# Performance work log

Hardware: AMD Instinct MI355X
Metric: run time of the kernel (lower is better)

## Reference

```python
import jax, jax.numpy as jnp
import numpy as np

B, I, N, T = 256, 1024, 1024, 100
TAU = 20.0
NUM_WEIGHT_BITS = 8  # -> numLsbBits = 8 - (8-1) = 1
VMAX = 2.0**23 - 1.0
VMIN = -(2.0**23) + 1.0


def setup_inputs() -> dict:
    key = jax.random.key(0)
    k1, k2, k3 = jax.random.split(key, 3)
    input_spikes = jax.random.randint(k1, (B, I, T), 0, 2, dtype=jnp.int32)  # binary spikes
    weight = jax.random.normal(k2, (N, I), dtype=jnp.float32)
    bias = jax.random.normal(k3, (N,), dtype=jnp.float32)
    return {"input_spikes": input_spikes, "weight": weight, "bias": bias}


def _quantize(weight, bias):
    # scale_factor = 255 / max|w|; int() truncates toward zero
    scale = 255.0 / jnp.max(jnp.abs(weight))
    qw = jnp.trunc(weight * scale)
    # (x >> 1) << 1 with arithmetic shift == floor(x/2)*2
    qw = jnp.floor(qw / 2.0) * 2.0
    qw = qw * 64.0
    qb = jnp.trunc(bias * scale) * 64.0
    vth = jnp.trunc(1.0 * scale) * 64.0  # vTh option default = 1.0
    return qw, qb, vth


def reference(input_spikes, weight, bias):
    qw, qb, vth = _quantize(weight, bias)
    decay = float(int(4096 - np.exp(-1.0 / TAU) * 4096))  # int truncation, = 199
    keep = (4096.0 - decay) / 4096.0
    spikes_t = jnp.transpose(input_spikes, (2, 0, 1)).astype(jnp.float32)  # [T,B,I]

    def step(v, s):
        wi = s @ qw.T                       # [B,N]
        v = v * keep + wi + qb              # soft LIF update
        v = jnp.clip(v, VMIN, VMAX)
        spike = (v >= vth).astype(jnp.float32)
        v = jnp.where(v > vth, v - vth, v)  # soft reset (strict >)
        return v, spike

    v0 = jnp.zeros((B, N), jnp.float32)
    _, spikes = jax.lax.scan(step, v0, spikes_t)       # [T,B,N]
    out = jnp.transpose(spikes, (1, 2, 0))             # [B,N,T]
    # delay == 1: prepend zeros, drop last two -> length T-1
    out = jnp.concatenate([jnp.zeros((B, N, 1), jnp.float32), out[..., : T - 2]], axis=-1)
    return out
```

## Files before the change

kernel.cpp:

```cpp
#include <hip/hip_runtime.h>
#include <hip/hip_bf16.h>
#include <stdint.h>

#define B_ 256
#define I_ 1024
#define N_ 1024
#define T_ 100
#define TP_ 128
#define TOUT 99
#define BN_ 64
#define KEEP (3897.0f/4096.0f)
#define VMAXF 8388607.0f
#define VMINF (-8388607.0f)

typedef __attribute__((ext_vector_type(8))) short short8;
typedef __attribute__((ext_vector_type(4))) float f32x4;

#define WS_MAX 0
#define WS_QB  4096
#define WS_QW  8192
#define WS_ST  (8192 + 2*1024*1024)

__global__ void maxabs_k(const float* __restrict__ w, unsigned* __restrict__ mx) {
  float m = 0.f;
  int stride = gridDim.x * blockDim.x;
  for (int i = blockIdx.x * blockDim.x + threadIdx.x; i < N_ * I_; i += stride)
    m = fmaxf(m, fabsf(w[i]));
  #pragma unroll
  for (int off = 32; off > 0; off >>= 1)
    m = fmaxf(m, __shfl_xor(m, off));
  if ((threadIdx.x & 63) == 0) atomicMax(mx, __float_as_uint(m));
}

__global__ void quant_k(const float* __restrict__ w, const float* __restrict__ bias,
                        const unsigned* __restrict__ mx,
                        unsigned short* __restrict__ qw, float* __restrict__ qb) {
  const float scale = 255.0f / __uint_as_float(*mx);
  int gid = blockIdx.x * blockDim.x + threadIdx.x;
  int stride = gridDim.x * blockDim.x;
  for (int idx = gid; idx < N_ * I_; idx += stride) {
    float q = truncf(__fmul_rn(w[idx], scale));
    q = floorf(q * 0.5f) * 2.0f;
    q = q * 64.0f;
    qw[idx] = (unsigned short)(__float_as_uint(q) >> 16);
  }
  if (gid < N_)
    qb[gid] = truncf(__fmul_rn(bias[gid], scale)) * 64.0f;
}

__global__ void spk_transpose_k(const int* __restrict__ spk, unsigned short* __restrict__ st) {
  __shared__ unsigned short tile[TP_][66];
  const int b = blockIdx.y;
  const int i0 = blockIdx.x * 64;
  for (int idx = threadIdx.x; idx < 28 * 64; idx += 256)
    tile[100 + (idx >> 6)][idx & 63] = 0;
  for (int idx = threadIdx.x; idx < 64 * 25; idx += 256) {
    int il = idx / 25, c = idx - il * 25;
    const int4 v = *(const int4*)(spk + ((size_t)(b * I_ + i0 + il)) * T_ + 4 * c);
    int t = 4 * c;
    tile[t + 0][il] = (unsigned short)(v.x ? 0x3F80 : 0);
    tile[t + 1][il] = (unsigned short)(v.y ? 0x3F80 : 0);
    tile[t + 2][il] = (unsigned short)(v.z ? 0x3F80 : 0);
    tile[t + 3][il] = (unsigned short)(v.w ? 0x3F80 : 0);
  }
  __syncthreads();
  for (int idx = threadIdx.x; idx < 128 * 32; idx += 256) {
    int t = idx >> 5, c = idx & 31;
    unsigned u = *(const unsigned*)&tile[t][c * 2];
    *(unsigned*)(st + ((size_t)b * TP_ + t) * I_ + i0 + c * 2) = u;
  }
}

__global__ __launch_bounds__(256, 4)
void gemm_scan_k(const unsigned short* __restrict__ st,
                 const unsigned short* __restrict__ qw,
                 const float* __restrict__ qb,
                 const unsigned* __restrict__ mx,
                 float* __restrict__ out) {
  __shared__ __align__(16) char smem[128 * 65 * 4];

  const int bid = blockIdx.x;
  const int swz = (bid & 7) * 512 + (bid >> 3);
  const int b  = swz >> 4;
  const int n0 = (swz & 15) * BN_;

  const int tid  = threadIdx.x;
  const int lane = tid & 63;
  const int wv   = tid >> 6;
  const int wr = wv >> 1, wc = wv & 1;
  const int lrow = lane & 15;
  const int lk16 = (lane >> 4) * 16;

  f32x4 acc[4][2];
  #pragma unroll
  for (int i = 0; i < 4; ++i)
    #pragma unroll
    for (int j = 0; j < 2; ++j)
      acc[i][j] = (f32x4){0.f, 0.f, 0.f, 0.f};

  const char* stB = (const char*)st + (size_t)b * TP_ * I_ * 2;
  const char* qwB = (const char*)qw + (size_t)n0 * I_ * 2;

  const char* gA[4]; const char* gB[2];
  #pragma unroll
  for (int j = 0; j < 4; ++j) {
    int lin = (j * 256 + tid) * 16;
    int row = lin >> 7, cb = lin & 127;
    gA[j] = stB + (size_t)row * 2048 + (cb ^ ((row & 7) << 4));
  }
  #pragma unroll
  for (int j = 0; j < 2; ++j) {
    int lin = (j * 256 + tid) * 16;
    int row = lin >> 7, cb = lin & 127;
    gB[j] = qwB + (size_t)row * 2048 + (cb ^ ((row & 7) << 4));
  }

  int offA[4][2], offB[2][2];
  #pragma unroll
  for (int mi = 0; mi < 4; ++mi) {
    int row = wr * 64 + mi * 16 + lrow;
    #pragma unroll
    for (int kk = 0; kk < 2; ++kk)
      offA[mi][kk] = row * 128 + ((kk * 64 + lk16) ^ ((row & 7) << 4));
  }
  #pragma unroll
  for (int ni = 0; ni < 2; ++ni) {
    int row = wc * 32 + ni * 16 + lrow;
    #pragma unroll
    for (int kk = 0; kk < 2; ++kk)
      offB[ni][kk] = 16384 + row * 128 + ((kk * 64 + lk16) ^ ((row & 7) << 4));
  }

  for (int ks = 0; ks < 16; ++ks) {
    const int g = ks * 128;
    #pragma unroll
    for (int j = 0; j < 4; ++j)
      __builtin_amdgcn_global_load_lds(
          (const __attribute__((address_space(1))) void*)(gA[j] + g),
          (__attribute__((address_space(3))) void*)(smem + j * 4096 + wv * 1024), 16, 0, 0);
    #pragma unroll
    for (int j = 0; j < 2; ++j)
      __builtin_amdgcn_global_load_lds(
          (const __attribute__((address_space(1))) void*)(gB[j] + g),
          (__attribute__((address_space(3))) void*)(smem + 16384 + j * 4096 + wv * 1024), 16, 0, 0);
    __syncthreads();

    #pragma unroll
    for (int kk = 0; kk < 2; ++kk) {
      short8 af[4], bf[2];
      #pragma unroll
      for (int mi = 0; mi < 4; ++mi) af[mi] = *(const short8*)(smem + offA[mi][kk]);
      #pragma unroll
      for (int ni = 0; ni < 2; ++ni) bf[ni] = *(const short8*)(smem + offB[ni][kk]);
      #pragma unroll
      for (int mi = 0; mi < 4; ++mi)
        #pragma unroll
        for (int ni = 0; ni < 2; ++ni)
          acc[mi][ni] = __builtin_amdgcn_mfma_f32_16x16x32_bf16(af[mi], bf[ni], acc[mi][ni], 0, 0, 0);
    }
    __syncthreads();
  }

  float* WI = (float*)smem;
  #pragma unroll
  for (int mi = 0; mi < 4; ++mi) {
    int row = wr * 64 + mi * 16 + (lane >> 4) * 4;
    #pragma unroll
    for (int ni = 0; ni < 2; ++ni) {
      int col = wc * 32 + ni * 16 + (lane & 15);
      #pragma unroll
      for (int j = 0; j < 4; ++j)
        WI[(row + j) * 65 + col] = acc[mi][ni][j];
    }
  }
  __syncthreads();

  if (tid < BN_) {
    const float scale = 255.0f / __uint_as_float(*mx);
    const float vth = truncf(scale) * 64.0f;
    const float qbn = qb[n0 + tid];
    float v = 0.f;
    float* orow = out + (size_t)(b * N_ + n0 + tid) * TOUT;
    orow[0] = 0.0f;
    for (int t = 0; t < 98; ++t) {
      float wi = WI[t * 65 + tid];
      v = __fadd_rn(__fadd_rn(__fmul_rn(v, KEEP), wi), qbn);
      v = fminf(fmaxf(v, VMINF), VMAXF);
      orow[t + 1] = (v >= vth) ? 1.0f : 0.0f;
      if (v > vth) v = __fsub_rn(v, vth);
    }
  }
}

extern "C" void kernel_launch(void* const* d_in, const int* in_sizes, int n_in,
                              void* d_out, int out_size, void* d_ws, size_t ws_size,
                              hipStream_t stream) {
  const int*   spikes = (const int*)d_in[0];
  const float* weight = (const float*)d_in[1];
  const float* bias   = (const float*)d_in[2];
  float* out = (float*)d_out;
  char* ws = (char*)d_ws;

  unsigned*       mx = (unsigned*)(ws + WS_MAX);
  float*          qb = (float*)(ws + WS_QB);
  unsigned short* qw = (unsigned short*)(ws + WS_QW);
  unsigned short* st = (unsigned short*)(ws + WS_ST);

  hipMemsetAsync(mx, 0, 4, stream);
  maxabs_k<<<256, 256, 0, stream>>>(weight, mx);
  quant_k<<<1024, 256, 0, stream>>>(weight, bias, mx, qw, qb);
  spk_transpose_k<<<dim3(16, 256), 256, 0, stream>>>(spikes, st);
  gemm_scan_k<<<4096, 256, 0, stream>>>(st, qw, qb, mx, out);
}
```

Before: 315.5 us.

## Switch spike GEMM to int8 MFMA with double-buffered LDS staging

Stores the quantized weights as int8 (floor(q/2)) and the spikes as int8 0/1, then runs the batched spike GEMM with i32 16x16x64 int8 MFMA and rescales by 128 in the epilogue. This halves the bytes for the weight and spike operands and doubles the K-step per MFMA. The main loop also double-buffers LDS, prefetching the next K tile while computing the current one, using explicit waitcnt and barriers. Integer accumulation stays exact because the products are small, but the hand-placed waitcnt and barrier ordering is fragile.

```diff
diff --git a/kernel.cpp b/kernel.cpp
--- a/kernel.cpp
+++ b/kernel.cpp
@@ -1,5 +1,4 @@
 #include <hip/hip_runtime.h>
-#include <hip/hip_bf16.h>
 #include <stdint.h>
 
 #define B_ 256
@@ -13,13 +12,12 @@
 #define VMAXF 8388607.0f
 #define VMINF (-8388607.0f)
 
-typedef __attribute__((ext_vector_type(8))) short short8;
-typedef __attribute__((ext_vector_type(4))) float f32x4;
+typedef __attribute__((ext_vector_type(4))) int i32x4;
 
 #define WS_MAX 0
 #define WS_QB  4096
 #define WS_QW  8192
-#define WS_ST  (8192 + 2*1024*1024)
+#define WS_ST  (8192 + 1024*1024 + 4096)
 
 __global__ void maxabs_k(const float* __restrict__ w, unsigned* __restrict__ mx) {
   float m = 0.f;
@@ -34,22 +32,20 @@
 
 __global__ void quant_k(const float* __restrict__ w, const float* __restrict__ bias,
                         const unsigned* __restrict__ mx,
-                        unsigned short* __restrict__ qw, float* __restrict__ qb) {
+                        signed char* __restrict__ qw, float* __restrict__ qb) {
   const float scale = 255.0f / __uint_as_float(*mx);
   int gid = blockIdx.x * blockDim.x + threadIdx.x;
   int stride = gridDim.x * blockDim.x;
   for (int idx = gid; idx < N_ * I_; idx += stride) {
-    float q = truncf(__fmul_rn(w[idx], scale));
-    q = floorf(q * 0.5f) * 2.0f;
-    q = q * 64.0f;
-    qw[idx] = (unsigned short)(__float_as_uint(q) >> 16);
+    int qi = (int)truncf(__fmul_rn(w[idx], scale));
+    qw[idx] = (signed char)(qi >> 1);
   }
   if (gid < N_)
     qb[gid] = truncf(__fmul_rn(bias[gid], scale)) * 64.0f;
 }
 
-__global__ void spk_transpose_k(const int* __restrict__ spk, unsigned short* __restrict__ st) {
-  __shared__ unsigned short tile[TP_][66];
+__global__ void spk_transpose_k(const int* __restrict__ spk, signed char* __restrict__ st) {
+  __shared__ unsigned char tile[TP_][80];
   const int b = blockIdx.y;
   const int i0 = blockIdx.x * 64;
   for (int idx = threadIdx.x; idx < 28 * 64; idx += 256)
@@ -58,22 +54,22 @@
     int il = idx / 25, c = idx - il * 25;
     const int4 v = *(const int4*)(spk + ((size_t)(b * I_ + i0 + il)) * T_ + 4 * c);
     int t = 4 * c;
-    tile[t + 0][il] = (unsigned short)(v.x ? 0x3F80 : 0);
-    tile[t + 1][il] = (unsigned short)(v.y ? 0x3F80 : 0);
-    tile[t + 2][il] = (unsigned short)(v.z ? 0x3F80 : 0);
-    tile[t + 3][il] = (unsigned short)(v.w ? 0x3F80 : 0);
+    tile[t + 0][il] = (unsigned char)v.x;
+    tile[t + 1][il] = (unsigned char)v.y;
+    tile[t + 2][il] = (unsigned char)v.z;
+    tile[t + 3][il] = (unsigned char)v.w;
   }
   __syncthreads();
-  for (int idx = threadIdx.x; idx < 128 * 32; idx += 256) {
-    int t = idx >> 5, c = idx & 31;
-    unsigned u = *(const unsigned*)&tile[t][c * 2];
-    *(unsigned*)(st + ((size_t)b * TP_ + t) * I_ + i0 + c * 2) = u;
+  for (int idx = threadIdx.x; idx < 128 * 4; idx += 256) {
+    int t = idx >> 2, q = idx & 3;
+    uint4 u = *(const uint4*)&tile[t][q * 16];
+    *(uint4*)(st + ((size_t)(b * 128 + t)) * I_ + i0 + q * 16) = u;
   }
 }
 
 __global__ __launch_bounds__(256, 4)
-void gemm_scan_k(const unsigned short* __restrict__ st,
-                 const unsigned short* __restrict__ qw,
+void gemm_scan_k(const signed char* __restrict__ st,
+                 const signed char* __restrict__ qw,
                  const float* __restrict__ qb,
                  const unsigned* __restrict__ mx,
                  float* __restrict__ out) {
@@ -89,77 +85,83 @@
   const int wv   = tid >> 6;
   const int wr = wv >> 1, wc = wv & 1;
   const int lrow = lane & 15;
-  const int lk16 = (lane >> 4) * 16;
-
-  f32x4 acc[4][2];
+  const int ls   = lane >> 4;
+
+  i32x4 acc[4][2];
   #pragma unroll
   for (int i = 0; i < 4; ++i)
     #pragma unroll
     for (int j = 0; j < 2; ++j)
-      acc[i][j] = (f32x4){0.f, 0.f, 0.f, 0.f};
-
-  const char* stB = (const char*)st + (size_t)b * TP_ * I_ * 2;
-  const char* qwB = (const char*)qw + (size_t)n0 * I_ * 2;
-
-  const char* gA[4]; const char* gB[2];
-  #pragma unroll
-  for (int j = 0; j < 4; ++j) {
-    int lin = (j * 256 + tid) * 16;
-    int row = lin >> 7, cb = lin & 127;
-    gA[j] = stB + (size_t)row * 2048 + (cb ^ ((row & 7) << 4));
-  }
+      acc[i][j] = (i32x4){0, 0, 0, 0};
+
+  const char* stB = (const char*)st + (size_t)b * TP_ * I_;
+  const char* qwB = (const char*)qw + (size_t)n0 * I_;
+
+  const char* gA[2]; const char* gB1;
   #pragma unroll
   for (int j = 0; j < 2; ++j) {
-    int lin = (j * 256 + tid) * 16;
-    int row = lin >> 7, cb = lin & 127;
-    gB[j] = qwB + (size_t)row * 2048 + (cb ^ ((row & 7) << 4));
-  }
-
-  int offA[4][2], offB[2][2];
+    int slot = j * 256 + tid;
+    int row = slot >> 2, s = slot & 3;
+    gA[j] = stB + (size_t)row * I_ + ((s ^ ((row >> 1) & 3)) << 4);
+  }
+  { int slot = tid;
+    int row = slot >> 2, s = slot & 3;
+    gB1 = qwB + (size_t)row * I_ + ((s ^ ((row >> 1) & 3)) << 4); }
+
+  int offA[4], offB[2];
   #pragma unroll
   for (int mi = 0; mi < 4; ++mi) {
     int row = wr * 64 + mi * 16 + lrow;
-    #pragma unroll
-    for (int kk = 0; kk < 2; ++kk)
-      offA[mi][kk] = row * 128 + ((kk * 64 + lk16) ^ ((row & 7) << 4));
+    offA[mi] = row * 64 + ((ls ^ ((row >> 1) & 3)) << 4);
   }
   #pragma unroll
   for (int ni = 0; ni < 2; ++ni) {
     int row = wc * 32 + ni * 16 + lrow;
-    #pragma unroll
-    for (int kk = 0; kk < 2; ++kk)
-      offB[ni][kk] = 16384 + row * 128 + ((kk * 64 + lk16) ^ ((row & 7) << 4));
-  }
-
+    offB[ni] = 8192 + row * 64 + ((ls ^ ((row >> 1) & 3)) << 4);
+  }
+
+  #define STAGE(bufbase, ksrc) do {                                                   \
+    const int g_ = (ksrc) * 64;                                                       \
+    __builtin_amdgcn_global_load_lds(                                                 \
+        (const __attribute__((address_space(1))) void*)(gA[0] + g_),                  \
+        (__attribute__((address_space(3))) void*)(smem + (bufbase) + wv * 1024), 16, 0, 0); \
+    __builtin_amdgcn_global_load_lds(                                                 \
+        (const __attribute__((address_space(1))) void*)(gA[1] + g_),                  \
+        (__attribute__((address_space(3))) void*)(smem + (bufbase) + 4096 + wv * 1024), 16, 0, 0); \
+    __builtin_amdgcn_global_load_lds(                                                 \
+        (const __attribute__((address_space(1))) void*)(gB1 + g_),                    \
+        (__attribute__((address_space(3))) void*)(smem + (bufbase) + 8192 + wv * 1024), 16, 0, 0); \
+  } while (0)
+
+  STAGE(0, 0);
+  int p = 0;
   for (int ks = 0; ks < 16; ++ks) {
-    const int g = ks * 128;
-    #pragma unroll
-    for (int j = 0; j < 4; ++j)
-      __builtin_amdgcn_global_load_lds(
-          (const __attribute__((address_space(1))) void*)(gA[j] + g),
-          (__attribute__((address_space(3))) void*)(smem + j * 4096 + wv * 1024), 16, 0, 0);
-    #pragma unroll
-    for (int j = 0; j < 2; ++j)
-      __builtin_amdgcn_global_load_lds(
-          (const __attribute__((address_space(1))) void*)(gB[j] + g),
-          (__attribute__((address_space(3))) void*)(smem + 16384 + j * 4096 + wv * 1024), 16, 0, 0);
-    __syncthreads();
-
-    #pragma unroll
-    for (int kk = 0; kk < 2; ++kk) {
-      short8 af[4], bf[2];
+    STAGE(12288 - p, (ks + 1) & 15);
+    __builtin_amdgcn_sched_barrier(0);
+    asm volatile("s_waitcnt vmcnt(3)" ::: "memory");
+    __builtin_amdgcn_s_barrier();
+    __builtin_amdgcn_sched_barrier(0);
+
+    i32x4 af[4], bf[2];
+    #pragma unroll
+    for (int mi = 0; mi < 4; ++mi) af[mi] = *(const i32x4*)(smem + p + offA[mi]);
+    #pragma unroll
+    for (int ni = 0; ni < 2; ++ni) bf[ni] = *(const i32x4*)(smem + p + offB[ni]);
+    asm volatile("s_waitcnt lgkmcnt(0)" ::: "memory");
+    __builtin_amdgcn_sched_barrier(0);
+    __builtin_amdgcn_s_barrier();
+
+    #pragma unroll
+    for (int mi = 0; mi < 4; ++mi)
       #pragma unroll
-      for (int mi = 0; mi < 4; ++mi) af[mi] = *(const short8*)(smem + offA[mi][kk]);
-      #pragma unroll
-      for (int ni = 0; ni < 2; ++ni) bf[ni] = *(const short8*)(smem + offB[ni][kk]);
-      #pragma unroll
-      for (int mi = 0; mi < 4; ++mi)
-        #pragma unroll
-        for (int ni = 0; ni < 2; ++ni)
-          acc[mi][ni] = __builtin_amdgcn_mfma_f32_16x16x32_bf16(af[mi], bf[ni], acc[mi][ni], 0, 0, 0);
-    }
-    __syncthreads();
-  }
+      for (int ni = 0; ni < 2; ++ni)
+        acc[mi][ni] = __builtin_amdgcn_mfma_i32_16x16x64_i8(af[mi], bf[ni], acc[mi][ni], 0, 0, 0);
+    p = 12288 - p;
+  }
+
+  asm volatile("s_waitcnt vmcnt(0)" ::: "memory");
+  __builtin_amdgcn_sched_barrier(0);
+  __builtin_amdgcn_s_barrier();
 
   float* WI = (float*)smem;
   #pragma unroll
@@ -170,7 +172,7 @@
       int col = wc * 32 + ni * 16 + (lane & 15);
       #pragma unroll
       for (int j = 0; j < 4; ++j)
-        WI[(row + j) * 65 + col] = acc[mi][ni][j];
+        WI[(row + j) * 65 + col] = 128.0f * (float)acc[mi][ni][j];
     }
   }
   __syncthreads();
@@ -201,10 +203,10 @@
   float* out = (float*)d_out;
   char* ws = (char*)d_ws;
 
-  unsigned*       mx = (unsigned*)(ws + WS_MAX);
-  float*          qb = (float*)(ws + WS_QB);
-  unsigned short* qw = (unsigned short*)(ws + WS_QW);
-  unsigned short* st = (unsigned short*)(ws + WS_ST);
+  unsigned*    mx = (unsigned*)(ws + WS_MAX);
+  float*       qb = (float*)(ws + WS_QB);
+  signed char* qw = (signed char*)(ws + WS_QW);
+  signed char* st = (signed char*)(ws + WS_ST);
 
   hipMemsetAsync(mx, 0, 4, stream);
   maxabs_k<<<256, 256, 0, stream>>>(weight, mx);
```

Result: faster. 298.0 us (-5.5%).
